# Performance work log

Hardware: AMD Instinct MI355X
Metric: run time of the kernel (lower is better)

The kernel has to match this reference:

```python
import jax, jax.numpy as jnp
import numpy as np

B, D, C = 4096, 128, 256


def setup_inputs() -> dict:
    key = jax.random.key(0)
    kx, km, kc = jax.random.split(key, 3)
    X = jax.random.normal(kx, (B, D), dtype=jnp.float32)
    means = jax.random.normal(km, (D, C), dtype=jnp.float32)
    # Build an SPD covariance and invert it (as the torch module does in __init__)
    A = jax.random.normal(kc, (D, D), dtype=jnp.float32)
    covar = A @ A.T / D + jnp.eye(D, dtype=jnp.float32)
    alpha = jnp.linalg.inv(covar)  # [D, D]
    return {"X": X, "means": means, "alpha": alpha}


def reference(X, means, alpha):
    # X: [B, D], means: [D, C], alpha: [D, D]
    d2 = X[:, :, None] - means[None, :, :]          # [B, D, C]
    # Quadratic form diagonal only: q[b,c] = d2[b,:,c]^T alpha d2[b,:,c]
    ad2 = jnp.einsum('de,bec->bdc', alpha, d2)       # [B, D, C]
    q = jnp.einsum('bdc,bdc->bc', d2, ad2)           # [B, C]
    return jnp.min(q, axis=1)                        # [B]
```

## Files before the change

### kernel.cpp

```cpp
#include <hip/hip_runtime.h>
#include <hip/hip_bf16.h>

constexpr int Bn = 4096;
constexpr int Dn = 128;
constexpr int Cn = 256;

typedef __attribute__((ext_vector_type(8))) short bf16x8;
typedef __attribute__((ext_vector_type(4))) float f32x4;

static __device__ inline unsigned short f2bfu(float f) {
    __hip_bfloat16 h = __float2bfloat16(f);
    return *reinterpret_cast<unsigned short*>(&h);
}
static __device__ inline float bfu2f(unsigned short u) {
    __hip_bfloat16 h = *reinterpret_cast<__hip_bfloat16*>(&u);
    return __bfloat162float(h);
}
static __device__ inline unsigned pk2(float x, float y) {
    return (unsigned)f2bfu(x) | ((unsigned)f2bfu(y) << 16);
}

#define SWZ_OFF(row, e) ((row) * 256 + ((((e) * 2)) ^ (((row) & 7) << 4)))

__global__ __launch_bounds__(512) void fused_kernel(
    const float* __restrict__ X, const float* __restrict__ means,
    const float* __restrict__ alpha, float* __restrict__ out) {
    __shared__ __align__(16) unsigned char AL[Dn * 256];
    __shared__ __align__(16) unsigned char MT[Cn * 256];
    __shared__ float TL[Cn];
    __shared__ float SMIN[8][16];
    __shared__ float SXAX[8][16];

    const int tid = threadIdx.x;
    const int w = tid >> 6;
    const int lane = tid & 63;
    const int l15 = lane & 15;
    const int lh = lane >> 4;
    const int b0 = blockIdx.x * 16;

    {
        const float4* a4 = (const float4*)alpha;
        #pragma unroll
        for (int i = 0; i < 8; ++i) {
            int idx4 = tid + i * 512;
            int d = idx4 >> 5, e0 = (idx4 & 31) << 2;
            float4 v = a4[idx4];
            unsigned char* p = AL + SWZ_OFF(d, e0);
            *(unsigned*)p = pk2(v.x, v.y);
            *(unsigned*)(p + 4) = pk2(v.z, v.w);
        }
        const int cb = 8 * w + (lane & 7);
        const int db0 = lane >> 3;
        #pragma unroll
        for (int i = 0; i < 4; ++i) {
            const int db = db0 + 8 * i;
            float4 v0 = *(const float4*)&means[(4 * db + 0) * Cn + 4 * cb];
            float4 v1 = *(const float4*)&means[(4 * db + 1) * Cn + 4 * cb];
            float4 v2 = *(const float4*)&means[(4 * db + 2) * Cn + 4 * cb];
            float4 v3 = *(const float4*)&means[(4 * db + 3) * Cn + 4 * cb];
            uint2 pk;
            pk.x = pk2(v0.x, v1.x); pk.y = pk2(v2.x, v3.x);
            *(uint2*)(MT + SWZ_OFF(4 * cb + 0, 4 * db)) = pk;
            pk.x = pk2(v0.y, v1.y); pk.y = pk2(v2.y, v3.y);
            *(uint2*)(MT + SWZ_OFF(4 * cb + 1, 4 * db)) = pk;
            pk.x = pk2(v0.z, v1.z); pk.y = pk2(v2.z, v3.z);
            *(uint2*)(MT + SWZ_OFF(4 * cb + 2, 4 * db)) = pk;
            pk.x = pk2(v0.w, v1.w); pk.y = pk2(v2.w, v3.w);
            *(uint2*)(MT + SWZ_OFF(4 * cb + 3, 4 * db)) = pk;
        }
    }
    __syncthreads();

    f32x4 gacc[2][8];
    #pragma unroll
    for (int j = 0; j < 2; ++j)
        #pragma unroll
        for (int mt = 0; mt < 8; ++mt) gacc[j][mt] = (f32x4){0.f, 0.f, 0.f, 0.f};

    #pragma unroll
    for (int k0 = 0; k0 < 4; ++k0) {
        bf16x8 bj[2];
        #pragma unroll
        for (int j = 0; j < 2; ++j) {
            const int c = 32 * w + 16 * j + l15;
            bj[j] = *(const bf16x8*)(MT + SWZ_OFF(c, 32 * k0 + 8 * lh));
        }
        #pragma unroll
        for (int mt = 0; mt < 8; ++mt) {
            bf16x8 a = *(const bf16x8*)(AL + SWZ_OFF(16 * mt + l15, 32 * k0 + 8 * lh));
            #pragma unroll
            for (int j = 0; j < 2; ++j)
                gacc[j][mt] = __builtin_amdgcn_mfma_f32_16x16x32_bf16(a, bj[j], gacc[j][mt], 0, 0, 0);
        }
    }

    {
        float tp[2];
        #pragma unroll
        for (int j = 0; j < 2; ++j) {
            const int c = 32 * w + 16 * j + l15;
            float v = 0.f;
            #pragma unroll
            for (int mt = 0; mt < 8; ++mt) {
                uint2 pk = *(const uint2*)(MT + SWZ_OFF(c, 16 * mt + 4 * lh));
                v = fmaf(bfu2f((unsigned short)(pk.x & 0xffffu)), gacc[j][mt][0], v);
                v = fmaf(bfu2f((unsigned short)(pk.x >> 16)),     gacc[j][mt][1], v);
                v = fmaf(bfu2f((unsigned short)(pk.y & 0xffffu)), gacc[j][mt][2], v);
                v = fmaf(bfu2f((unsigned short)(pk.y >> 16)),     gacc[j][mt][3], v);
            }
            v += __shfl_xor(v, 16);
            v += __shfl_xor(v, 32);
            tp[j] = v;
        }
        if (lane < 16) {
            TL[32 * w + lane] = tp[0];
            TL[32 * w + 16 + lane] = tp[1];
        }
    }
    __syncthreads();

    #pragma unroll
    for (int j = 0; j < 2; ++j) {
        const int c = 32 * w + 16 * j + l15;
        #pragma unroll
        for (int mt = 0; mt < 8; ++mt) {
            uint2 pk;
            pk.x = pk2(gacc[j][mt][0], gacc[j][mt][1]);
            pk.y = pk2(gacc[j][mt][2], gacc[j][mt][3]);
            *(uint2*)(MT + SWZ_OFF(c, 16 * mt + 4 * lh)) = pk;
        }
    }
    __syncthreads();

    bf16x8 af[4];
    {
        const float* xrow = X + (b0 + l15) * Dn;
        #pragma unroll
        for (int k0 = 0; k0 < 4; ++k0) {
            const float4* p = (const float4*)(xrow + 32 * k0 + 8 * lh);
            float4 x0 = p[0], x1 = p[1];
            bf16x8 a;
            a[0] = (short)f2bfu(x0.x); a[1] = (short)f2bfu(x0.y);
            a[2] = (short)f2bfu(x0.z); a[3] = (short)f2bfu(x0.w);
            a[4] = (short)f2bfu(x1.x); a[5] = (short)f2bfu(x1.y);
            a[6] = (short)f2bfu(x1.z); a[7] = (short)f2bfu(x1.w);
            af[k0] = a;
        }
    }
    bf16x8 bf3[3][4];
    #pragma unroll
    for (int j2 = 0; j2 < 3; ++j2) {
        const int tg = 3 * w + j2;
        const unsigned char* base = (tg < 16) ? (const unsigned char*)MT : (const unsigned char*)AL;
        const int rowc = (tg < 16) ? (16 * tg + l15) : (16 * (tg - 16) + l15);
        #pragma unroll
        for (int k0 = 0; k0 < 4; ++k0)
            bf3[j2][k0] = *(const bf16x8*)(base + SWZ_OFF(rowc, 32 * k0 + 8 * lh));
    }
    f32x4 macc[3];
    #pragma unroll
    for (int j2 = 0; j2 < 3; ++j2) macc[j2] = (f32x4){0.f, 0.f, 0.f, 0.f};
    #pragma unroll
    for (int k0 = 0; k0 < 4; ++k0)
        #pragma unroll
        for (int j2 = 0; j2 < 3; ++j2)
            macc[j2] = __builtin_amdgcn_mfma_f32_16x16x32_bf16(af[k0], bf3[j2][k0], macc[j2], 0, 0, 0);

    {
        float mr[4], px[4];
        #pragma unroll
        for (int r = 0; r < 4; ++r) { mr[r] = 1e30f; px[r] = 0.f; }
        #pragma unroll
        for (int j2 = 0; j2 < 3; ++j2) {
            const int tg = 3 * w + j2;
            if (tg < 16) {
                float tc = TL[16 * tg + l15];
                #pragma unroll
                for (int r = 0; r < 4; ++r)
                    mr[r] = fminf(mr[r], tc - 2.f * macc[j2][r]);
            } else {
                const int dp = 16 * (tg - 16) + l15;
                #pragma unroll
                for (int r = 0; r < 4; ++r)
                    px[r] = fmaf(macc[j2][r], X[(b0 + 4 * lh + r) * Dn + dp], px[r]);
            }
        }
        #pragma unroll
        for (int r = 0; r < 4; ++r) {
            #pragma unroll
            for (int m = 1; m < 16; m <<= 1) {
                mr[r] = fminf(mr[r], __shfl_xor(mr[r], m));
                px[r] += __shfl_xor(px[r], m);
            }
        }
        if (l15 == 0) {
            #pragma unroll
            for (int r = 0; r < 4; ++r) {
                SMIN[w][4 * lh + r] = mr[r];
                SXAX[w][4 * lh + r] = px[r];
            }
        }
    }
    __syncthreads();

    if (tid < 16) {
        float mnv = 1e30f, xa = 0.f;
        #pragma unroll
        for (int w8 = 0; w8 < 8; ++w8) {
            mnv = fminf(mnv, SMIN[w8][tid]);
            xa += SXAX[w8][tid];
        }
        out[b0 + tid] = xa + mnv;
    }
}

extern "C" void kernel_launch(void* const* d_in, const int* in_sizes, int n_in,
                              void* d_out, int out_size, void* d_ws, size_t ws_size,
                              hipStream_t stream) {
    const float* X     = (const float*)d_in[0];
    const float* means = (const float*)d_in[1];
    const float* alpha = (const float*)d_in[2];
    float* out = (float*)d_out;
    fused_kernel<<<Bn / 16, 512, 0, stream>>>(X, means, alpha, out);
}
```

Baseline: 13.49 us.

## Stage X tile in LDS, compute x^T A x in first GEMM phase, drop sync

Loads the block's 16 rows of X once into swizzled bf16 LDS and computes the x^T·alpha·x term with an extra MFMA per k-step during the alpha·means phase. This rebalances the second phase so each wave handles two centroid tiles instead of three mixed tiles. The per-centroid constant now stays in registers instead of going through a TL LDS array, which removes one __syncthreads. It also removes the scattered global reads of X in the epilogue. In exchange it adds a small amount of LDS and extra MFMA work in phase one.

Result: faster. 11.73 us (-13.1%).

```diff
diff --git a/kernel.cpp b/kernel.cpp
--- a/kernel.cpp
+++ b/kernel.cpp
@@ -27,7 +27,7 @@
     const float* __restrict__ alpha, float* __restrict__ out) {
     __shared__ __align__(16) unsigned char AL[Dn * 256];
     __shared__ __align__(16) unsigned char MT[Cn * 256];
-    __shared__ float TL[Cn];
+    __shared__ __align__(16) unsigned char XL[16 * 256];
     __shared__ float SMIN[8][16];
     __shared__ float SXAX[8][16];
 
@@ -39,6 +39,14 @@
     const int b0 = blockIdx.x * 16;
 
     {
+        {
+            float4 v = ((const float4*)(X + b0 * Dn))[tid];
+            const int b = tid >> 5;
+            const int e0 = (tid & 31) << 2;
+            uint2 pk;
+            pk.x = pk2(v.x, v.y); pk.y = pk2(v.z, v.w);
+            *(uint2*)(XL + SWZ_OFF(b, e0)) = pk;
+        }
         const float4* a4 = (const float4*)alpha;
         #pragma unroll
         for (int i = 0; i < 8; ++i) {
@@ -76,6 +84,7 @@
     for (int j = 0; j < 2; ++j)
         #pragma unroll
         for (int mt = 0; mt < 8; ++mt) gacc[j][mt] = (f32x4){0.f, 0.f, 0.f, 0.f};
+    f32x4 xacc = (f32x4){0.f, 0.f, 0.f, 0.f};
 
     #pragma unroll
     for (int k0 = 0; k0 < 4; ++k0) {
@@ -92,32 +101,41 @@
             for (int j = 0; j < 2; ++j)
                 gacc[j][mt] = __builtin_amdgcn_mfma_f32_16x16x32_bf16(a, bj[j], gacc[j][mt], 0, 0, 0);
         }
+        {
+            bf16x8 a = *(const bf16x8*)(AL + SWZ_OFF(16 * w + l15, 32 * k0 + 8 * lh));
+            bf16x8 bx = *(const bf16x8*)(XL + SWZ_OFF(l15, 32 * k0 + 8 * lh));
+            xacc = __builtin_amdgcn_mfma_f32_16x16x32_bf16(a, bx, xacc, 0, 0, 0);
+        }
     }
 
     {
-        float tp[2];
-        #pragma unroll
-        for (int j = 0; j < 2; ++j) {
-            const int c = 32 * w + 16 * j + l15;
-            float v = 0.f;
-            #pragma unroll
-            for (int mt = 0; mt < 8; ++mt) {
-                uint2 pk = *(const uint2*)(MT + SWZ_OFF(c, 16 * mt + 4 * lh));
-                v = fmaf(bfu2f((unsigned short)(pk.x & 0xffffu)), gacc[j][mt][0], v);
-                v = fmaf(bfu2f((unsigned short)(pk.x >> 16)),     gacc[j][mt][1], v);
-                v = fmaf(bfu2f((unsigned short)(pk.y & 0xffffu)), gacc[j][mt][2], v);
-                v = fmaf(bfu2f((unsigned short)(pk.y >> 16)),     gacc[j][mt][3], v);
-            }
-            v += __shfl_xor(v, 16);
-            v += __shfl_xor(v, 32);
-            tp[j] = v;
-        }
-        if (lane < 16) {
-            TL[32 * w + lane] = tp[0];
-            TL[32 * w + 16 + lane] = tp[1];
-        }
-    }
-    __syncthreads();
+        uint2 pk = *(const uint2*)(XL + SWZ_OFF(l15, 16 * w + 4 * lh));
+        float v = bfu2f((unsigned short)(pk.x & 0xffffu)) * xacc[0];
+        v = fmaf(bfu2f((unsigned short)(pk.x >> 16)),     xacc[1], v);
+        v = fmaf(bfu2f((unsigned short)(pk.y & 0xffffu)), xacc[2], v);
+        v = fmaf(bfu2f((unsigned short)(pk.y >> 16)),     xacc[3], v);
+        v += __shfl_xor(v, 16);
+        v += __shfl_xor(v, 32);
+        if (lane < 16) SXAX[w][lane] = v;
+    }
+
+    float tp[2];
+    #pragma unroll
+    for (int j = 0; j < 2; ++j) {
+        const int c = 32 * w + 16 * j + l15;
+        float v = 0.f;
+        #pragma unroll
+        for (int mt = 0; mt < 8; ++mt) {
+            uint2 pk = *(const uint2*)(MT + SWZ_OFF(c, 16 * mt + 4 * lh));
+            v = fmaf(bfu2f((unsigned short)(pk.x & 0xffffu)), gacc[j][mt][0], v);
+            v = fmaf(bfu2f((unsigned short)(pk.x >> 16)),     gacc[j][mt][1], v);
+            v = fmaf(bfu2f((unsigned short)(pk.y & 0xffffu)), gacc[j][mt][2], v);
+            v = fmaf(bfu2f((unsigned short)(pk.y >> 16)),     gacc[j][mt][3], v);
+        }
+        v += __shfl_xor(v, 16);
+        v += __shfl_xor(v, 32);
+        tp[j] = v;
+    }
 
     #pragma unroll
     for (int j = 0; j < 2; ++j) {
@@ -133,73 +151,46 @@
     __syncthreads();
 
     bf16x8 af[4];
+    #pragma unroll
+    for (int k0 = 0; k0 < 4; ++k0)
+        af[k0] = *(const bf16x8*)(XL + SWZ_OFF(l15, 32 * k0 + 8 * lh));
+    bf16x8 bf2[2][4];
+    #pragma unroll
+    for (int j2 = 0; j2 < 2; ++j2) {
+        const int rowc = 16 * (2 * w + j2) + l15;
+        #pragma unroll
+        for (int k0 = 0; k0 < 4; ++k0)
+            bf2[j2][k0] = *(const bf16x8*)(MT + SWZ_OFF(rowc, 32 * k0 + 8 * lh));
+    }
+    f32x4 macc[2];
+    #pragma unroll
+    for (int j2 = 0; j2 < 2; ++j2) macc[j2] = (f32x4){0.f, 0.f, 0.f, 0.f};
+    #pragma unroll
+    for (int k0 = 0; k0 < 4; ++k0)
+        #pragma unroll
+        for (int j2 = 0; j2 < 2; ++j2)
+            macc[j2] = __builtin_amdgcn_mfma_f32_16x16x32_bf16(af[k0], bf2[j2][k0], macc[j2], 0, 0, 0);
+
     {
-        const float* xrow = X + (b0 + l15) * Dn;
-        #pragma unroll
-        for (int k0 = 0; k0 < 4; ++k0) {
-            const float4* p = (const float4*)(xrow + 32 * k0 + 8 * lh);
-            float4 x0 = p[0], x1 = p[1];
-            bf16x8 a;
-            a[0] = (short)f2bfu(x0.x); a[1] = (short)f2bfu(x0.y);
-            a[2] = (short)f2bfu(x0.z); a[3] = (short)f2bfu(x0.w);
-            a[4] = (short)f2bfu(x1.x); a[5] = (short)f2bfu(x1.y);
-            a[6] = (short)f2bfu(x1.z); a[7] = (short)f2bfu(x1.w);
-            af[k0] = a;
-        }
-    }
-    bf16x8 bf3[3][4];
-    #pragma unroll
-    for (int j2 = 0; j2 < 3; ++j2) {
-        const int tg = 3 * w + j2;
-        const unsigned char* base = (tg < 16) ? (const unsigned char*)MT : (const unsigned char*)AL;
-        const int rowc = (tg < 16) ? (16 * tg + l15) : (16 * (tg - 16) + l15);
-        #pragma unroll
-        for (int k0 = 0; k0 < 4; ++k0)
-            bf3[j2][k0] = *(const bf16x8*)(base + SWZ_OFF(rowc, 32 * k0 + 8 * lh));
-    }
-    f32x4 macc[3];
-    #pragma unroll
-    for (int j2 = 0; j2 < 3; ++j2) macc[j2] = (f32x4){0.f, 0.f, 0.f, 0.f};
-    #pragma unroll
-    for (int k0 = 0; k0 < 4; ++k0)
-        #pragma unroll
-        for (int j2 = 0; j2 < 3; ++j2)
-            macc[j2] = __builtin_amdgcn_mfma_f32_16x16x32_bf16(af[k0], bf3[j2][k0], macc[j2], 0, 0, 0);
-
-    {
-        float mr[4], px[4];
-        #pragma unroll
-        for (int r = 0; r < 4; ++r) { mr[r] = 1e30f; px[r] = 0.f; }
-        #pragma unroll
-        for (int j2 = 0; j2 < 3; ++j2) {
-            const int tg = 3 * w + j2;
-            if (tg < 16) {
-                float tc = TL[16 * tg + l15];
-                #pragma unroll
-                for (int r = 0; r < 4; ++r)
-                    mr[r] = fminf(mr[r], tc - 2.f * macc[j2][r]);
-            } else {
-                const int dp = 16 * (tg - 16) + l15;
-                #pragma unroll
-                for (int r = 0; r < 4; ++r)
-                    px[r] = fmaf(macc[j2][r], X[(b0 + 4 * lh + r) * Dn + dp], px[r]);
-            }
+        float mr[4];
+        #pragma unroll
+        for (int r = 0; r < 4; ++r) mr[r] = 1e30f;
+        #pragma unroll
+        for (int j2 = 0; j2 < 2; ++j2) {
+            const float tc = tp[j2];
+            #pragma unroll
+            for (int r = 0; r < 4; ++r)
+                mr[r] = fminf(mr[r], tc - 2.f * macc[j2][r]);
         }
         #pragma unroll
         for (int r = 0; r < 4; ++r) {
             #pragma unroll
-            for (int m = 1; m < 16; m <<= 1) {
+            for (int m = 1; m < 16; m <<= 1)
                 mr[r] = fminf(mr[r], __shfl_xor(mr[r], m));
-                px[r] += __shfl_xor(px[r], m);
-            }
-        }
-        if (l15 == 0) {
-            #pragma unroll
-            for (int r = 0; r < 4; ++r) {
-                SMIN[w][4 * lh + r] = mr[r];
-                SXAX[w][4 * lh + r] = px[r];
-            }
-        }
+        }
+        if (l15 == 0)
+            #pragma unroll
+            for (int r = 0; r < 4; ++r) SMIN[w][4 * lh + r] = mr[r];
     }
     __syncthreads();
 
```

## Split batch-invariant alpha·means precompute into a separate setup kernel

Applied to the files above, without the earlier changes.

The work that does not depend on the batch (alpha·means in bf16, the per-class constant t_c, and the bf16 copy of alpha) moves out of every block and into a small setup kernel with 16 blocks. It writes a combined W matrix and a tvec array to the workspace. Before, each of the 256 blocks redid the full 128x256x128 GEMM and the conversions. The main kernel now only loads X into LDS and reads W straight from global memory. The cost is a second kernel launch and a dependency between the two kernels, and px now uses the bf16-rounded X instead of fp32.

After: 16.23 us. 20.3% more time.

```diff
diff --git a/kernel.cpp b/kernel.cpp
--- a/kernel.cpp
+++ b/kernel.cpp
@@ -4,6 +4,7 @@
 constexpr int Bn = 4096;
 constexpr int Dn = 128;
 constexpr int Cn = 256;
+constexpr int Wr = Cn + Dn;
 
 typedef __attribute__((ext_vector_type(8))) short bf16x8;
 typedef __attribute__((ext_vector_type(4))) float f32x4;
@@ -22,21 +23,30 @@
 
 #define SWZ_OFF(row, e) ((row) * 256 + ((((e) * 2)) ^ (((row) & 7) << 4)))
 
-__global__ __launch_bounds__(512) void fused_kernel(
-    const float* __restrict__ X, const float* __restrict__ means,
-    const float* __restrict__ alpha, float* __restrict__ out) {
+__global__ __launch_bounds__(512) void setup_kernel(
+    const float* __restrict__ means, const float* __restrict__ alpha,
+    unsigned short* __restrict__ W, float* __restrict__ tvec) {
+    const int tid = threadIdx.x;
+
+    if ((int)blockIdx.x >= 8) {
+        const int r0 = ((int)blockIdx.x - 8) * 16;
+        const int d = tid >> 5;
+        const int e0 = (tid & 31) << 2;
+        float4 v = *(const float4*)&alpha[(r0 + d) * Dn + e0];
+        unsigned* p = (unsigned*)&W[(Cn + r0 + d) * Dn + e0];
+        p[0] = pk2(v.x, v.y);
+        p[1] = pk2(v.z, v.w);
+        return;
+    }
+
     __shared__ __align__(16) unsigned char AL[Dn * 256];
-    __shared__ __align__(16) unsigned char MT[Cn * 256];
-    __shared__ float TL[Cn];
-    __shared__ float SMIN[8][16];
-    __shared__ float SXAX[8][16];
-
-    const int tid = threadIdx.x;
-    const int w = tid >> 6;
+    __shared__ __align__(16) unsigned char MTl[32 * 256];
+    __shared__ float TP[2][16][4];
+    const int cbase = (int)blockIdx.x * 32;
     const int lane = tid & 63;
     const int l15 = lane & 15;
     const int lh = lane >> 4;
-    const int b0 = blockIdx.x * 16;
+    const int w = tid >> 6;
 
     {
         const float4* a4 = (const float4*)alpha;
@@ -49,114 +59,104 @@
             *(unsigned*)p = pk2(v.x, v.y);
             *(unsigned*)(p + 4) = pk2(v.z, v.w);
         }
-        const int cb = 8 * w + (lane & 7);
-        const int db0 = lane >> 3;
-        #pragma unroll
-        for (int i = 0; i < 4; ++i) {
-            const int db = db0 + 8 * i;
-            float4 v0 = *(const float4*)&means[(4 * db + 0) * Cn + 4 * cb];
-            float4 v1 = *(const float4*)&means[(4 * db + 1) * Cn + 4 * cb];
-            float4 v2 = *(const float4*)&means[(4 * db + 2) * Cn + 4 * cb];
-            float4 v3 = *(const float4*)&means[(4 * db + 3) * Cn + 4 * cb];
-            uint2 pk;
-            pk.x = pk2(v0.x, v1.x); pk.y = pk2(v2.x, v3.x);
-            *(uint2*)(MT + SWZ_OFF(4 * cb + 0, 4 * db)) = pk;
-            pk.x = pk2(v0.y, v1.y); pk.y = pk2(v2.y, v3.y);
-            *(uint2*)(MT + SWZ_OFF(4 * cb + 1, 4 * db)) = pk;
-            pk.x = pk2(v0.z, v1.z); pk.y = pk2(v2.z, v3.z);
-            *(uint2*)(MT + SWZ_OFF(4 * cb + 2, 4 * db)) = pk;
-            pk.x = pk2(v0.w, v1.w); pk.y = pk2(v2.w, v3.w);
-            *(uint2*)(MT + SWZ_OFF(4 * cb + 3, 4 * db)) = pk;
-        }
-    }
-    __syncthreads();
-
-    f32x4 gacc[2][8];
-    #pragma unroll
-    for (int j = 0; j < 2; ++j)
-        #pragma unroll
-        for (int mt = 0; mt < 8; ++mt) gacc[j][mt] = (f32x4){0.f, 0.f, 0.f, 0.f};
-
+    }
+    if (tid < 256) {
+        const int cbl = tid & 7;
+        const int db = tid >> 3;
+        float4 v0 = *(const float4*)&means[(4 * db + 0) * Cn + cbase + 4 * cbl];
+        float4 v1 = *(const float4*)&means[(4 * db + 1) * Cn + cbase + 4 * cbl];
+        float4 v2 = *(const float4*)&means[(4 * db + 2) * Cn + cbase + 4 * cbl];
+        float4 v3 = *(const float4*)&means[(4 * db + 3) * Cn + cbase + 4 * cbl];
+        uint2 pk;
+        pk.x = pk2(v0.x, v1.x); pk.y = pk2(v2.x, v3.x);
+        *(uint2*)(MTl + SWZ_OFF(4 * cbl + 0, 4 * db)) = pk;
+        pk.x = pk2(v0.y, v1.y); pk.y = pk2(v2.y, v3.y);
+        *(uint2*)(MTl + SWZ_OFF(4 * cbl + 1, 4 * db)) = pk;
+        pk.x = pk2(v0.z, v1.z); pk.y = pk2(v2.z, v3.z);
+        *(uint2*)(MTl + SWZ_OFF(4 * cbl + 2, 4 * db)) = pk;
+        pk.x = pk2(v0.w, v1.w); pk.y = pk2(v2.w, v3.w);
+        *(uint2*)(MTl + SWZ_OFF(4 * cbl + 3, 4 * db)) = pk;
+    }
+    __syncthreads();
+
+    const int ct = w & 1, q = w >> 1;
+    f32x4 acc[2];
+    acc[0] = (f32x4){0.f, 0.f, 0.f, 0.f};
+    acc[1] = (f32x4){0.f, 0.f, 0.f, 0.f};
     #pragma unroll
     for (int k0 = 0; k0 < 4; ++k0) {
-        bf16x8 bj[2];
-        #pragma unroll
-        for (int j = 0; j < 2; ++j) {
-            const int c = 32 * w + 16 * j + l15;
-            bj[j] = *(const bf16x8*)(MT + SWZ_OFF(c, 32 * k0 + 8 * lh));
-        }
-        #pragma unroll
-        for (int mt = 0; mt < 8; ++mt) {
-            bf16x8 a = *(const bf16x8*)(AL + SWZ_OFF(16 * mt + l15, 32 * k0 + 8 * lh));
-            #pragma unroll
-            for (int j = 0; j < 2; ++j)
-                gacc[j][mt] = __builtin_amdgcn_mfma_f32_16x16x32_bf16(a, bj[j], gacc[j][mt], 0, 0, 0);
-        }
-    }
+        bf16x8 b = *(const bf16x8*)(MTl + SWZ_OFF(16 * ct + l15, 32 * k0 + 8 * lh));
+        #pragma unroll
+        for (int s = 0; s < 2; ++s) {
+            bf16x8 a = *(const bf16x8*)(AL + SWZ_OFF(16 * (2 * q + s) + l15, 32 * k0 + 8 * lh));
+            acc[s] = __builtin_amdgcn_mfma_f32_16x16x32_bf16(a, b, acc[s], 0, 0, 0);
+        }
+    }
+    const int c = cbase + 16 * ct + l15;
+    float tpart = 0.f;
+    #pragma unroll
+    for (int s = 0; s < 2; ++s) {
+        const int mt = 2 * q + s;
+        uint2 mm = *(const uint2*)(MTl + SWZ_OFF(16 * ct + l15, 16 * mt + 4 * lh));
+        tpart = fmaf(bfu2f((unsigned short)(mm.x & 0xffffu)), acc[s][0], tpart);
+        tpart = fmaf(bfu2f((unsigned short)(mm.x >> 16)),     acc[s][1], tpart);
+        tpart = fmaf(bfu2f((unsigned short)(mm.y & 0xffffu)), acc[s][2], tpart);
+        tpart = fmaf(bfu2f((unsigned short)(mm.y >> 16)),     acc[s][3], tpart);
+        uint2 pk;
+        pk.x = pk2(acc[s][0], acc[s][1]);
+        pk.y = pk2(acc[s][2], acc[s][3]);
+        *(uint2*)&W[c * Dn + 16 * mt + 4 * lh] = pk;
+    }
+    tpart += __shfl_xor(tpart, 16);
+    tpart += __shfl_xor(tpart, 32);
+    if (lane < 16) TP[ct][l15][q] = tpart;
+    __syncthreads();
+    if (tid < 32)
+        tvec[cbase + tid] = TP[tid >> 4][tid & 15][0] + TP[tid >> 4][tid & 15][1] +
+                            TP[tid >> 4][tid & 15][2] + TP[tid >> 4][tid & 15][3];
+}
+
+__global__ __launch_bounds__(512) void main_kernel(
+    const float* __restrict__ X, const unsigned short* __restrict__ W,
+    const float* __restrict__ tvec, float* __restrict__ out) {
+    __shared__ __align__(16) unsigned char XL[16 * 256];
+    __shared__ float SMIN[8][16];
+    __shared__ float SXAX[8][16];
+
+    const int tid = threadIdx.x;
+    const int w = tid >> 6;
+    const int lane = tid & 63;
+    const int l15 = lane & 15;
+    const int lh = lane >> 4;
+    const int b0 = blockIdx.x * 16;
 
     {
-        float tp[2];
-        #pragma unroll
-        for (int j = 0; j < 2; ++j) {
-            const int c = 32 * w + 16 * j + l15;
-            float v = 0.f;
-            #pragma unroll
-            for (int mt = 0; mt < 8; ++mt) {
-                uint2 pk = *(const uint2*)(MT + SWZ_OFF(c, 16 * mt + 4 * lh));
-                v = fmaf(bfu2f((unsigned short)(pk.x & 0xffffu)), gacc[j][mt][0], v);
-                v = fmaf(bfu2f((unsigned short)(pk.x >> 16)),     gacc[j][mt][1], v);
-                v = fmaf(bfu2f((unsigned short)(pk.y & 0xffffu)), gacc[j][mt][2], v);
-                v = fmaf(bfu2f((unsigned short)(pk.y >> 16)),     gacc[j][mt][3], v);
-            }
-            v += __shfl_xor(v, 16);
-            v += __shfl_xor(v, 32);
-            tp[j] = v;
-        }
-        if (lane < 16) {
-            TL[32 * w + lane] = tp[0];
-            TL[32 * w + 16 + lane] = tp[1];
-        }
-    }
-    __syncthreads();
-
-    #pragma unroll
-    for (int j = 0; j < 2; ++j) {
-        const int c = 32 * w + 16 * j + l15;
-        #pragma unroll
-        for (int mt = 0; mt < 8; ++mt) {
-            uint2 pk;
-            pk.x = pk2(gacc[j][mt][0], gacc[j][mt][1]);
-            pk.y = pk2(gacc[j][mt][2], gacc[j][mt][3]);
-            *(uint2*)(MT + SWZ_OFF(c, 16 * mt + 4 * lh)) = pk;
-        }
-    }
-    __syncthreads();
-
-    bf16x8 af[4];
-    {
-        const float* xrow = X + (b0 + l15) * Dn;
-        #pragma unroll
-        for (int k0 = 0; k0 < 4; ++k0) {
-            const float4* p = (const float4*)(xrow + 32 * k0 + 8 * lh);
-            float4 x0 = p[0], x1 = p[1];
-            bf16x8 a;
-            a[0] = (short)f2bfu(x0.x); a[1] = (short)f2bfu(x0.y);
-            a[2] = (short)f2bfu(x0.z); a[3] = (short)f2bfu(x0.w);
-            a[4] = (short)f2bfu(x1.x); a[5] = (short)f2bfu(x1.y);
-            a[6] = (short)f2bfu(x1.z); a[7] = (short)f2bfu(x1.w);
-            af[k0] = a;
-        }
-    }
-    bf16x8 bf3[3][4];
+        float4 v = ((const float4*)(X + b0 * Dn))[tid];
+        const int b = tid >> 5;
+        const int e0 = (tid & 31) << 2;
+        uint2 pk;
+        pk.x = pk2(v.x, v.y); pk.y = pk2(v.z, v.w);
+        *(uint2*)(XL + SWZ_OFF(b, e0)) = pk;
+    }
+
+    bf16x8 bfr[3][4];
+    float tcv[3];
     #pragma unroll
     for (int j2 = 0; j2 < 3; ++j2) {
         const int tg = 3 * w + j2;
-        const unsigned char* base = (tg < 16) ? (const unsigned char*)MT : (const unsigned char*)AL;
-        const int rowc = (tg < 16) ? (16 * tg + l15) : (16 * (tg - 16) + l15);
+        const unsigned short* wrow = W + (16 * tg + l15) * Dn;
         #pragma unroll
         for (int k0 = 0; k0 < 4; ++k0)
-            bf3[j2][k0] = *(const bf16x8*)(base + SWZ_OFF(rowc, 32 * k0 + 8 * lh));
-    }
+            bfr[j2][k0] = *(const bf16x8*)(wrow + 32 * k0 + 8 * lh);
+        tcv[j2] = (tg < 16) ? tvec[16 * tg + l15] : 0.f;
+    }
+    __syncthreads();
+
+    bf16x8 af[4];
+    #pragma unroll
+    for (int k0 = 0; k0 < 4; ++k0)
+        af[k0] = *(const bf16x8*)(XL + SWZ_OFF(l15, 32 * k0 + 8 * lh));
+
     f32x4 macc[3];
     #pragma unroll
     for (int j2 = 0; j2 < 3; ++j2) macc[j2] = (f32x4){0.f, 0.f, 0.f, 0.f};
@@ -164,7 +164,7 @@
     for (int k0 = 0; k0 < 4; ++k0)
         #pragma unroll
         for (int j2 = 0; j2 < 3; ++j2)
-            macc[j2] = __builtin_amdgcn_mfma_f32_16x16x32_bf16(af[k0], bf3[j2][k0], macc[j2], 0, 0, 0);
+            macc[j2] = __builtin_amdgcn_mfma_f32_16x16x32_bf16(af[k0], bfr[j2][k0], macc[j2], 0, 0, 0);
 
     {
         float mr[4], px[4];
@@ -174,15 +174,16 @@
         for (int j2 = 0; j2 < 3; ++j2) {
             const int tg = 3 * w + j2;
             if (tg < 16) {
-                float tc = TL[16 * tg + l15];
                 #pragma unroll
                 for (int r = 0; r < 4; ++r)
-                    mr[r] = fminf(mr[r], tc - 2.f * macc[j2][r]);
+                    mr[r] = fminf(mr[r], tcv[j2] - 2.f * macc[j2][r]);
             } else {
-                const int dp = 16 * (tg - 16) + l15;
+                const int d = 16 * (tg - 16) + l15;
                 #pragma unroll
-                for (int r = 0; r < 4; ++r)
-                    px[r] = fmaf(macc[j2][r], X[(b0 + 4 * lh + r) * Dn + dp], px[r]);
+                for (int r = 0; r < 4; ++r) {
+                    unsigned short u = *(const unsigned short*)(XL + SWZ_OFF(4 * lh + r, d));
+                    px[r] = fmaf(macc[j2][r], bfu2f(u), px[r]);
+                }
             }
         }
         #pragma unroll
@@ -221,5 +222,9 @@
     const float* means = (const float*)d_in[1];
     const float* alpha = (const float*)d_in[2];
     float* out = (float*)d_out;
-    fused_kernel<<<Bn / 16, 512, 0, stream>>>(X, means, alpha, out);
-}
+    unsigned short* W = (unsigned short*)d_ws;
+    float* tvec = (float*)((char*)d_ws + Wr * Dn * sizeof(unsigned short));
+
+    setup_kernel<<<16, 512, 0, stream>>>(means, alpha, W, tvec);
+    main_kernel<<<Bn / 16, 512, 0, stream>>>(X, W, tvec, out);
+}
```
